# Kernel tuning notes

Measured on AMD Instinct MI355X. Metric: run time of the kernel, lower is better.

Reference implementation:

```python
import jax, jax.numpy as jnp
import numpy as np

N, C, G = 262144, 256, 1024
R = C // 4  # reduction bottleneck


def _linear_w(key, out_dim, in_dim):
    # torch.nn.Linear default init: U(-1/sqrt(in), 1/sqrt(in)), weight shape [out, in]
    bound = 1.0 / np.sqrt(in_dim)
    return jax.random.uniform(key, (out_dim, in_dim), jnp.float32, -bound, bound)


def setup_inputs() -> dict:
    key = jax.random.key(0)
    ks = jax.random.split(key, 8)
    return {
        "x": jax.random.normal(ks[0], (N, C), jnp.float32),
        "glb_w1": _linear_w(ks[1], R, C),
        "glb_a": jnp.full((1,), 0.25, jnp.float32),   # PReLU param (default init 0.25)
        "glb_w2": _linear_w(ks[2], C, R),
        "local_w1": _linear_w(ks[3], R, C),
        "local_a": jnp.full((1,), 0.25, jnp.float32),
        "local_w2": _linear_w(ks[4], C, R),
        "attn_w1": _linear_w(ks[5], R, C),
        "attn_a": jnp.full((1,), 0.25, jnp.float32),
        "attn_w2": _linear_w(ks[6], C, R),
        "batch_idx": jnp.sort(jax.random.randint(ks[7], (N,), 0, G)),
        "num_graphs": G,
    }


def _mlp(h, w1, a, w2):
    # Linear(no bias) -> PReLU -> Linear(no bias)
    z = jnp.einsum('nc,rc->nr', h, w1)
    z = jnp.where(z >= 0, z, a * z)
    return jnp.einsum('nr,cr->nc', z, w2)


def reference(x, glb_w1, glb_a, glb_w2, local_w1, local_a, local_w2,
              attn_w1, attn_a, attn_w2, batch_idx, num_graphs):
    g = _mlp(x, glb_w1, glb_a, glb_w2)                                  # [N, C]
    seg_sum = jax.ops.segment_sum(g, batch_idx, num_segments=num_graphs)  # [G, C]
    cnt = jax.ops.segment_sum(jnp.ones((x.shape[0], 1), x.dtype), batch_idx,
                              num_segments=num_graphs)                  # [G, 1]
    seg_mean = seg_sum / jnp.maximum(cnt, 1.0)  # scatter_mean (0 for empty graphs)
    x_glb = seg_mean[batch_idx]                                          # gather back [N, C]
    loc = _mlp(x, local_w1, local_a, local_w2)                           # [N, C]
    attn = _mlp(loc + x_glb, attn_w1, attn_a, attn_w2)
    return jax.nn.sigmoid(attn)
```

## Files before the change

kernel.cpp:

```cpp
#include <hip/hip_runtime.h>

typedef unsigned short u16;
typedef __attribute__((ext_vector_type(8))) short short8;
typedef __attribute__((ext_vector_type(4))) float f32x4;
typedef __attribute__((ext_vector_type(4))) unsigned short u16x4;
typedef __attribute__((ext_vector_type(2))) unsigned u32x2;

#define NN 262144
#define CC 256
#define RR 64
#define GG 1024

#define SWZ(b, n) ((b) ^ (((n) & 7) << 4))
#define SSWZ(b, r) ((b) ^ (((r) & 7) << 4))


static __device__ __forceinline__ u16 f2bf(float f) {
  unsigned u = __builtin_bit_cast(unsigned, f);
  u += 0x7fffu + ((u >> 16) & 1u);
  return (u16)(u >> 16);
}

static __device__ __forceinline__ unsigned cvt_pk_bf16(float lo, float hi) {
  unsigned r;
  asm("v_cvt_pk_bf16_f32 %0, %1, %2" : "=v"(r) : "v"(lo), "v"(hi));
  return r;
}

static __device__ __forceinline__ void lgkm0() {
  __asm__ volatile("s_waitcnt lgkmcnt(0)" ::: "memory");
}

#define MFMA16(a, b, c) __builtin_amdgcn_mfma_f32_16x16x32_bf16((a), (b), (c), 0, 0, 0)

__global__ void k_prep(const float* __restrict__ a0, const float* __restrict__ a1,
                       const float* __restrict__ a2, const float* __restrict__ a3,
                       const float* __restrict__ a4, const float* __restrict__ a5,
                       u16* __restrict__ dst, float* __restrict__ zbase) {
  int bid = blockIdx.x;
  if (bid < 96) {
    int m = bid >> 4;
    const float* s = (m == 0) ? a0 : (m == 1) ? a1 : (m == 2) ? a2
                   : (m == 3) ? a3 : (m == 4) ? a4 : a5;
    int off = (((bid & 15) << 8) | threadIdx.x) << 2;
    f32x4 v = *(const f32x4*)(s + off);
    u16x4 p;
    p[0] = f2bf(v[0]); p[1] = f2bf(v[1]); p[2] = f2bf(v[2]); p[3] = f2bf(v[3]);
    *(u16x4*)(dst + m * 16384 + off) = p;
  } else {
    int idx = (bid - 96) * 256 + threadIdx.x;
    ((f32x4*)zbase)[idx] = (f32x4){0.f, 0.f, 0.f, 0.f};
  }
}

#define ZBOFF 16384

__global__ __launch_bounds__(256)
__attribute__((amdgpu_waves_per_eu(8, 8))) void k_glb(
    const float* __restrict__ x, const u16* __restrict__ wbf,
    const int* __restrict__ bidx, const float* __restrict__ pa,
    float* __restrict__ seg, int* __restrict__ cnt) {
  __shared__ __align__(16) char smem[20480];
  const int tid = threadIdx.x;
  const int wave = tid >> 6, lane = tid & 63;
  const int low = lane & 15, quad = lane >> 4;
  const int node0 = blockIdx.x << 5;
  const float alpha = pa[0];
  const u16* w1 = wbf;
  const u16* w2 = wbf + 16384;

  const int lbv = bidx[node0 + (lane & 31)];

  const float* xsrc = x + (size_t)node0 * CC;
#pragma unroll
  for (int k = 0; k < 8; k++) {
    int f = k * 1024 + tid * 4;
    f32x4 v = *(const f32x4*)(xsrc + f);
    int node = f >> 8;
    u32x2 p;
    p[0] = cvt_pk_bf16(v[0], v[1]);
    p[1] = cvt_pk_bf16(v[2], v[3]);
    *(u32x2*)(smem + SWZ(node * 512 + (f & 255) * 2, node)) = p;
  }

  if (wave == 0) {
    int cur = __shfl(lbv, 0), rl = 0;
#pragma unroll
    for (int n = 0; n < 32; n++) {
      int b = __shfl(lbv, n);
      if (b != cur) { if (lane == 0) atomicAdd(cnt + cur, rl); rl = 0; cur = b; }
      rl++;
    }
    if (lane == 0) atomicAdd(cnt + cur, rl);
  }
  __syncthreads();

  f32x4 z[2] = {};
  const u16* w1p = w1 + (wave * 16 + low) * CC;
#pragma unroll
  for (int ks = 0; ks < 8; ks++) {
    short8 wa = *(const short8*)(w1p + ks * 32 + quad * 8);
#pragma unroll
    for (int nt = 0; nt < 2; nt++) {
      int node = nt * 16 + low;
      short8 xf = *(const short8*)(smem + SWZ(node * 512 + ks * 64 + quad * 16, node));
      z[nt] = MFMA16(wa, xf, z[nt]);
    }
  }
#pragma unroll
  for (int nt = 0; nt < 2; nt++) {
    float v0 = z[nt][0], v1 = z[nt][1], v2 = z[nt][2], v3 = z[nt][3];
    v0 = v0 >= 0.f ? v0 : alpha * v0;
    v1 = v1 >= 0.f ? v1 : alpha * v1;
    v2 = v2 >= 0.f ? v2 : alpha * v2;
    v3 = v3 >= 0.f ? v3 : alpha * v3;
    int node = nt * 16 + low;
    u32x2 p;
    p[0] = cvt_pk_bf16(v0, v1);
    p[1] = cvt_pk_bf16(v2, v3);
    *(u32x2*)(smem + ZBOFF + SWZ(node * 128 + wave * 32 + quad * 8, node)) = p;
  }
  __syncthreads();

  char* slab = smem + wave * 4096;
#pragma unroll
  for (int nt = 0; nt < 2; nt++) {
    int node = nt * 16 + low;
    f32x4 g[4] = {};
#pragma unroll
    for (int ks2 = 0; ks2 < 2; ks2++) {
      short8 zf = *(const short8*)(smem + ZBOFF + SWZ(node * 128 + ks2 * 64 + quad * 16, node));
#pragma unroll
      for (int mt = 0; mt < 4; mt++) {
        short8 wa = *(const short8*)(w2 + (wave * 64 + mt * 16 + low) * RR + ks2 * 32 + quad * 8);
        g[mt] = MFMA16(wa, zf, g[mt]);
      }
    }
#pragma unroll
    for (int mt = 0; mt < 4; mt++)
      *(f32x4*)(slab + SSWZ(low * 256 + mt * 64 + quad * 16, low)) = g[mt];
    lgkm0();
    float acc = 0.f;
    int cur = __shfl(lbv, nt * 16);
#pragma unroll
    for (int n = 0; n < 16; n++) {
      int b = __shfl(lbv, nt * 16 + n);
      if (b != cur) {
        atomicAdd(seg + (size_t)cur * CC + wave * 64 + lane, acc);
        acc = 0.f; cur = b;
      }
      acc += *(const float*)(slab + SSWZ(n * 256 + lane * 4, n));
    }
    atomicAdd(seg + (size_t)cur * CC + wave * 64 + lane, acc);
    lgkm0();
  }
}

__global__ __launch_bounds__(256)
__attribute__((amdgpu_waves_per_eu(8, 8))) void k_attn(
    const float* __restrict__ x, const u16* __restrict__ wbf,
    const int* __restrict__ bidx, const float* __restrict__ seg,
    const int* __restrict__ cnt,
    const float* __restrict__ pal, const float* __restrict__ paa,
    float* __restrict__ out) {
  __shared__ __align__(16) char smem[20480];
  const int tid = threadIdx.x;
  const int wave = tid >> 6, lane = tid & 63;
  const int low = lane & 15, quad = lane >> 4;
  const int node0 = blockIdx.x << 5;
  const float al = pal[0], aa = paa[0];
  const u16* w1l = wbf + 2 * 16384;
  const u16* w2l = wbf + 3 * 16384;
  const u16* w1a = wbf + 4 * 16384;
  const u16* w2a = wbf + 5 * 16384;

  int bb[2], cc[2];
#pragma unroll
  for (int nt = 0; nt < 2; nt++) bb[nt] = bidx[node0 + nt * 16 + low];
#pragma unroll
  for (int nt = 0; nt < 2; nt++) cc[nt] = cnt[bb[nt]];

  const float* xsrc = x + (size_t)node0 * CC;
#pragma unroll
  for (int k = 0; k < 8; k++) {
    int f = k * 1024 + tid * 4;
    f32x4 v = *(const f32x4*)(xsrc + f);
    int node = f >> 8;
    u32x2 p;
    p[0] = cvt_pk_bf16(v[0], v[1]);
    p[1] = cvt_pk_bf16(v[2], v[3]);
    *(u32x2*)(smem + SWZ(node * 512 + (f & 255) * 2, node)) = p;
  }
  __syncthreads();

  f32x4 z[2] = {};
  const u16* w1p = w1l + (wave * 16 + low) * CC;
#pragma unroll
  for (int ks = 0; ks < 8; ks++) {
    short8 wa = *(const short8*)(w1p + ks * 32 + quad * 8);
#pragma unroll
    for (int nt = 0; nt < 2; nt++) {
      int node = nt * 16 + low;
      short8 xf = *(const short8*)(smem + SWZ(node * 512 + ks * 64 + quad * 16, node));
      z[nt] = MFMA16(wa, xf, z[nt]);
    }
  }
#pragma unroll
  for (int nt = 0; nt < 2; nt++) {
    float v0 = z[nt][0], v1 = z[nt][1], v2 = z[nt][2], v3 = z[nt][3];
    v0 = v0 >= 0.f ? v0 : al * v0;
    v1 = v1 >= 0.f ? v1 : al * v1;
    v2 = v2 >= 0.f ? v2 : al * v2;
    v3 = v3 >= 0.f ? v3 : al * v3;
    int node = nt * 16 + low;
    u32x2 p;
    p[0] = cvt_pk_bf16(v0, v1);
    p[1] = cvt_pk_bf16(v2, v3);
    *(u32x2*)(smem + ZBOFF + SWZ(node * 128 + wave * 32 + quad * 8, node)) = p;
  }
  __syncthreads();

#pragma unroll
  for (int nt = 0; nt < 2; nt++) {
    int node = nt * 16 + low;
    f32x4 loc[4] = {};
#pragma unroll
    for (int ks2 = 0; ks2 < 2; ks2++) {
      short8 zf = *(const short8*)(smem + ZBOFF + SWZ(node * 128 + ks2 * 64 + quad * 16, node));
#pragma unroll
      for (int mt = 0; mt < 4; mt++) {
        short8 wa = *(const short8*)(w2l + (wave * 64 + mt * 16 + low) * RR + ks2 * 32 + quad * 8);
        loc[mt] = MFMA16(wa, zf, loc[mt]);
      }
    }
    const float* srow = seg + (size_t)bb[nt] * CC + wave * 64;
    float inv = (cc[nt] > 0) ? __builtin_amdgcn_rcpf((float)cc[nt]) : 0.0f;
#pragma unroll
    for (int mt = 0; mt < 4; mt++) {
      f32x4 sv = *(const f32x4*)(srow + mt * 16 + quad * 4);
      u32x2 p;
      p[0] = cvt_pk_bf16(fmaf(sv[0], inv, loc[mt][0]),
                         fmaf(sv[1], inv, loc[mt][1]));
      p[1] = cvt_pk_bf16(fmaf(sv[2], inv, loc[mt][2]),
                         fmaf(sv[3], inv, loc[mt][3]));
      *(u32x2*)(smem + SWZ(node * 512 + wave * 128 + mt * 32 + quad * 8, node)) = p;
    }
  }
  __syncthreads();

  f32x4 z2[2] = {};
  const u16* w1pa = w1a + (wave * 16 + low) * CC;
#pragma unroll
  for (int ks = 0; ks < 8; ks++) {
    short8 wa = *(const short8*)(w1pa + ks * 32 + quad * 8);
#pragma unroll
    for (int nt = 0; nt < 2; nt++) {
      int node = nt * 16 + low;
      short8 hf = *(const short8*)(smem + SWZ(node * 512 + ks * 64 + quad * 16, node));
      z2[nt] = MFMA16(wa, hf, z2[nt]);
    }
  }
#pragma unroll
  for (int nt = 0; nt < 2; nt++) {
    float v0 = z2[nt][0], v1 = z2[nt][1], v2 = z2[nt][2], v3 = z2[nt][3];
    v0 = v0 >= 0.f ? v0 : aa * v0;
    v1 = v1 >= 0.f ? v1 : aa * v1;
    v2 = v2 >= 0.f ? v2 : aa * v2;
    v3 = v3 >= 0.f ? v3 : aa * v3;
    int node = nt * 16 + low;
    u32x2 p;
    p[0] = cvt_pk_bf16(v0, v1);
    p[1] = cvt_pk_bf16(v2, v3);
    *(u32x2*)(smem + ZBOFF + SWZ(node * 128 + wave * 32 + quad * 8, node)) = p;
  }
  __syncthreads();

#pragma unroll
  for (int nt = 0; nt < 2; nt++) {
    int node = nt * 16 + low;
    f32x4 o[4] = {};
#pragma unroll
    for (int ks2 = 0; ks2 < 2; ks2++) {
      short8 zf = *(const short8*)(smem + ZBOFF + SWZ(node * 128 + ks2 * 64 + quad * 16, node));
#pragma unroll
      for (int mt = 0; mt < 4; mt++) {
        short8 wa = *(const short8*)(w2a + (wave * 64 + mt * 16 + low) * RR + ks2 * 32 + quad * 8);
        o[mt] = MFMA16(wa, zf, o[mt]);
      }
    }
    float* orow = out + (size_t)(node0 + node) * CC + wave * 64;
#pragma unroll
    for (int mt = 0; mt < 4; mt++) {
#pragma unroll
      for (int i = 0; i < 4; i++)
        o[mt][i] = __builtin_amdgcn_rcpf(1.0f + __expf(-o[mt][i]));
      *(f32x4*)(orow + mt * 16 + quad * 4) = o[mt];
    }
  }
}

extern "C" void kernel_launch(void* const* d_in, const int* in_sizes, int n_in,
                              void* d_out, int out_size, void* d_ws, size_t ws_size,
                              hipStream_t stream) {
  (void)in_sizes; (void)n_in; (void)out_size; (void)ws_size;
  const float* x   = (const float*)d_in[0];
  const float* w1g = (const float*)d_in[1];
  const float* ag  = (const float*)d_in[2];
  const float* w2g = (const float*)d_in[3];
  const float* w1l = (const float*)d_in[4];
  const float* al  = (const float*)d_in[5];
  const float* w2l = (const float*)d_in[6];
  const float* w1a = (const float*)d_in[7];
  const float* aa  = (const float*)d_in[8];
  const float* w2a = (const float*)d_in[9];
  const int* bidx  = (const int*)d_in[10];
  float* out = (float*)d_out;

  u16* wbf   = (u16*)d_ws;
  float* seg = (float*)((char*)d_ws + 196608);
  int* cnt   = (int*)((char*)d_ws + 196608 + 1048576);

  k_prep<<<353, 256, 0, stream>>>(w1g, w2g, w1l, w2l, w1a, w2a, wbf, seg);
  k_glb<<<NN / 32, 256, 0, stream>>>(x, wbf, bidx, ag, seg, cnt);
  k_attn<<<NN / 32, 256, 0, stream>>>(x, wbf, bidx, seg, cnt, al, aa, out);
}
```

Measured before the change: 683.8 us.

## Fuse phases into persistent cooperative kernel with bf16 x cache and prefetch

Replaces the three launches with one persistent cooperative kernel of 1280 blocks that uses grid syncs between weight conversion, the global MLP with segment-sum, and the attention phase. During the global phase each block writes the bf16-converted x tile to workspace, so the attention phase reads half as many bytes instead of re-reading fp32 x. Both tile loops prefetch the next tile's x and batch indices into registers while the current tile computes, and occupancy is pinned to 5 waves per EU. Risks are grid-sync cost, reduced occupancy, and dependence on workspace size, with a three-launch fallback when cooperative launch is unavailable.

```diff
diff --git a/kernel.cpp b/kernel.cpp
--- a/kernel.cpp
+++ b/kernel.cpp
@@ -1,4 +1,7 @@
 #include <hip/hip_runtime.h>
+#include <hip/hip_cooperative_groups.h>
+
+namespace cg = cooperative_groups;
 
 typedef unsigned short u16;
 typedef __attribute__((ext_vector_type(8))) short short8;
@@ -10,10 +13,15 @@
 #define CC 256
 #define RR 64
 #define GG 1024
+#define NTILES 8192
+#define NB 1280
 
 #define SWZ(b, n) ((b) ^ (((n) & 7) << 4))
 #define SSWZ(b, r) ((b) ^ (((r) & 7) << 4))
 
+#define XBFOFF 1249280
+#define XBFSZ  ((size_t)NN * CC * 2)
+#define ZBOFF 16384
 
 static __device__ __forceinline__ u16 f2bf(float f) {
   unsigned u = __builtin_bit_cast(unsigned, f);
@@ -33,268 +41,301 @@
 
 #define MFMA16(a, b, c) __builtin_amdgcn_mfma_f32_16x16x32_bf16((a), (b), (c), 0, 0, 0)
 
-__global__ void k_prep(const float* __restrict__ a0, const float* __restrict__ a1,
-                       const float* __restrict__ a2, const float* __restrict__ a3,
-                       const float* __restrict__ a4, const float* __restrict__ a5,
-                       u16* __restrict__ dst, float* __restrict__ zbase) {
-  int bid = blockIdx.x;
-  if (bid < 96) {
-    int m = bid >> 4;
-    const float* s = (m == 0) ? a0 : (m == 1) ? a1 : (m == 2) ? a2
-                   : (m == 3) ? a3 : (m == 4) ? a4 : a5;
-    int off = (((bid & 15) << 8) | threadIdx.x) << 2;
-    f32x4 v = *(const f32x4*)(s + off);
-    u16x4 p;
-    p[0] = f2bf(v[0]); p[1] = f2bf(v[1]); p[2] = f2bf(v[2]); p[3] = f2bf(v[3]);
-    *(u16x4*)(dst + m * 16384 + off) = p;
-  } else {
-    int idx = (bid - 96) * 256 + threadIdx.x;
-    ((f32x4*)zbase)[idx] = (f32x4){0.f, 0.f, 0.f, 0.f};
-  }
-}
-
-#define ZBOFF 16384
-
 __global__ __launch_bounds__(256)
-__attribute__((amdgpu_waves_per_eu(8, 8))) void k_glb(
-    const float* __restrict__ x, const u16* __restrict__ wbf,
-    const int* __restrict__ bidx, const float* __restrict__ pa,
-    float* __restrict__ seg, int* __restrict__ cnt) {
+__attribute__((amdgpu_waves_per_eu(5, 5))) void k_main(
+    int phase,
+    const float* __restrict__ x, u16* __restrict__ wbf,
+    const float* __restrict__ ws0, const float* __restrict__ ws1,
+    const float* __restrict__ ws2, const float* __restrict__ ws3,
+    const float* __restrict__ ws4, const float* __restrict__ ws5,
+    const int* __restrict__ bidx,
+    const float* __restrict__ pag, const float* __restrict__ pal,
+    const float* __restrict__ paa,
+    float* __restrict__ seg, int* __restrict__ cnt,
+    char* __restrict__ xbf, float* __restrict__ out) {
   __shared__ __align__(16) char smem[20480];
   const int tid = threadIdx.x;
   const int wave = tid >> 6, lane = tid & 63;
   const int low = lane & 15, quad = lane >> 4;
-  const int node0 = blockIdx.x << 5;
-  const float alpha = pa[0];
-  const u16* w1 = wbf;
-  const u16* w2 = wbf + 16384;
-
-  const int lbv = bidx[node0 + (lane & 31)];
-
-  const float* xsrc = x + (size_t)node0 * CC;
-#pragma unroll
-  for (int k = 0; k < 8; k++) {
-    int f = k * 1024 + tid * 4;
-    f32x4 v = *(const f32x4*)(xsrc + f);
-    int node = f >> 8;
-    u32x2 p;
-    p[0] = cvt_pk_bf16(v[0], v[1]);
-    p[1] = cvt_pk_bf16(v[2], v[3]);
-    *(u32x2*)(smem + SWZ(node * 512 + (f & 255) * 2, node)) = p;
-  }
-
-  if (wave == 0) {
-    int cur = __shfl(lbv, 0), rl = 0;
-#pragma unroll
-    for (int n = 0; n < 32; n++) {
-      int b = __shfl(lbv, n);
-      if (b != cur) { if (lane == 0) atomicAdd(cnt + cur, rl); rl = 0; cur = b; }
-      rl++;
-    }
-    if (lane == 0) atomicAdd(cnt + cur, rl);
-  }
-  __syncthreads();
-
-  f32x4 z[2] = {};
-  const u16* w1p = w1 + (wave * 16 + low) * CC;
-#pragma unroll
-  for (int ks = 0; ks < 8; ks++) {
-    short8 wa = *(const short8*)(w1p + ks * 32 + quad * 8);
-#pragma unroll
-    for (int nt = 0; nt < 2; nt++) {
-      int node = nt * 16 + low;
-      short8 xf = *(const short8*)(smem + SWZ(node * 512 + ks * 64 + quad * 16, node));
-      z[nt] = MFMA16(wa, xf, z[nt]);
-    }
-  }
-#pragma unroll
-  for (int nt = 0; nt < 2; nt++) {
-    float v0 = z[nt][0], v1 = z[nt][1], v2 = z[nt][2], v3 = z[nt][3];
-    v0 = v0 >= 0.f ? v0 : alpha * v0;
-    v1 = v1 >= 0.f ? v1 : alpha * v1;
-    v2 = v2 >= 0.f ? v2 : alpha * v2;
-    v3 = v3 >= 0.f ? v3 : alpha * v3;
-    int node = nt * 16 + low;
-    u32x2 p;
-    p[0] = cvt_pk_bf16(v0, v1);
-    p[1] = cvt_pk_bf16(v2, v3);
-    *(u32x2*)(smem + ZBOFF + SWZ(node * 128 + wave * 32 + quad * 8, node)) = p;
-  }
-  __syncthreads();
-
-  char* slab = smem + wave * 4096;
-#pragma unroll
-  for (int nt = 0; nt < 2; nt++) {
-    int node = nt * 16 + low;
-    f32x4 g[4] = {};
-#pragma unroll
-    for (int ks2 = 0; ks2 < 2; ks2++) {
-      short8 zf = *(const short8*)(smem + ZBOFF + SWZ(node * 128 + ks2 * 64 + quad * 16, node));
-#pragma unroll
-      for (int mt = 0; mt < 4; mt++) {
-        short8 wa = *(const short8*)(w2 + (wave * 64 + mt * 16 + low) * RR + ks2 * 32 + quad * 8);
-        g[mt] = MFMA16(wa, zf, g[mt]);
-      }
-    }
-#pragma unroll
-    for (int mt = 0; mt < 4; mt++)
-      *(f32x4*)(slab + SSWZ(low * 256 + mt * 64 + quad * 16, low)) = g[mt];
-    lgkm0();
-    float acc = 0.f;
-    int cur = __shfl(lbv, nt * 16);
-#pragma unroll
-    for (int n = 0; n < 16; n++) {
-      int b = __shfl(lbv, nt * 16 + n);
-      if (b != cur) {
+
+  if (phase == 0 || phase == 3) {
+    int idx = blockIdx.x * 256 + tid;
+    if (idx < 24576) {
+      int m = idx >> 12, o4 = (idx & 4095) << 2;
+      const float* s = (m == 0) ? ws0 : (m == 1) ? ws1 : (m == 2) ? ws2
+                     : (m == 3) ? ws3 : (m == 4) ? ws4 : ws5;
+      f32x4 v = *(const f32x4*)(s + o4);
+      u16x4 p;
+      p[0] = f2bf(v[0]); p[1] = f2bf(v[1]); p[2] = f2bf(v[2]); p[3] = f2bf(v[3]);
+      *(u16x4*)(wbf + m * 16384 + o4) = p;
+    } else if (idx < 24576 + 65792) {
+      ((f32x4*)seg)[idx - 24576] = (f32x4){0.f, 0.f, 0.f, 0.f};
+    }
+  }
+  if (phase == 3) cg::this_grid().sync();
+
+  if (phase == 1 || phase == 3) {
+    const u16* w1 = wbf;
+    const u16* w2 = wbf + 16384;
+    const float alpha = pag[0];
+    f32x4 xn[8];
+    int lbvn = 0;
+    int t0 = blockIdx.x;
+    if (t0 < NTILES) {
+      const float* xs = x + ((size_t)t0 << 5) * CC;
+#pragma unroll
+      for (int k = 0; k < 8; k++) xn[k] = *(const f32x4*)(xs + k * 1024 + tid * 4);
+      lbvn = bidx[(t0 << 5) + (lane & 31)];
+    }
+    for (int t = t0; t < NTILES; t += gridDim.x) {
+      const int lbv = lbvn;
+      char* xtile = xbf ? (xbf + ((size_t)t << 14)) : nullptr;
+#pragma unroll
+      for (int k = 0; k < 8; k++) {
+        int f = k * 1024 + tid * 4;
+        int node = f >> 8;
+        u32x2 p;
+        p[0] = cvt_pk_bf16(xn[k][0], xn[k][1]);
+        p[1] = cvt_pk_bf16(xn[k][2], xn[k][3]);
+        int off = SWZ(node * 512 + (f & 255) * 2, node);
+        *(u32x2*)(smem + off) = p;
+        if (xtile) *(u32x2*)(xtile + off) = p;
+      }
+      __syncthreads();
+      if (t + (int)gridDim.x < NTILES) {
+        const float* xs = x + ((size_t)(t + gridDim.x) << 5) * CC;
+#pragma unroll
+        for (int k = 0; k < 8; k++) xn[k] = *(const f32x4*)(xs + k * 1024 + tid * 4);
+        lbvn = bidx[((t + gridDim.x) << 5) + (lane & 31)];
+      }
+      if (wave == 0) {
+        int cur = __shfl(lbv, 0), rl = 0;
+#pragma unroll
+        for (int n = 0; n < 32; n++) {
+          int b = __shfl(lbv, n);
+          if (b != cur) { if (lane == 0) atomicAdd(cnt + cur, rl); rl = 0; cur = b; }
+          rl++;
+        }
+        if (lane == 0) atomicAdd(cnt + cur, rl);
+      }
+      f32x4 z[2] = {};
+      const u16* w1p = w1 + (wave * 16 + low) * CC;
+#pragma unroll
+      for (int ks = 0; ks < 8; ks++) {
+        short8 wa = *(const short8*)(w1p + ks * 32 + quad * 8);
+#pragma unroll
+        for (int nt = 0; nt < 2; nt++) {
+          int node = nt * 16 + low;
+          short8 xf = *(const short8*)(smem + SWZ(node * 512 + ks * 64 + quad * 16, node));
+          z[nt] = MFMA16(wa, xf, z[nt]);
+        }
+      }
+#pragma unroll
+      for (int nt = 0; nt < 2; nt++) {
+        float v0 = z[nt][0], v1 = z[nt][1], v2 = z[nt][2], v3 = z[nt][3];
+        v0 = v0 >= 0.f ? v0 : alpha * v0;
+        v1 = v1 >= 0.f ? v1 : alpha * v1;
+        v2 = v2 >= 0.f ? v2 : alpha * v2;
+        v3 = v3 >= 0.f ? v3 : alpha * v3;
+        int node = nt * 16 + low;
+        u32x2 p;
+        p[0] = cvt_pk_bf16(v0, v1);
+        p[1] = cvt_pk_bf16(v2, v3);
+        *(u32x2*)(smem + ZBOFF + SWZ(node * 128 + wave * 32 + quad * 8, node)) = p;
+      }
+      __syncthreads();
+      char* slab = smem + wave * 4096;
+#pragma unroll
+      for (int nt = 0; nt < 2; nt++) {
+        int node = nt * 16 + low;
+        f32x4 g[4] = {};
+#pragma unroll
+        for (int ks2 = 0; ks2 < 2; ks2++) {
+          short8 zf = *(const short8*)(smem + ZBOFF + SWZ(node * 128 + ks2 * 64 + quad * 16, node));
+#pragma unroll
+          for (int mt = 0; mt < 4; mt++) {
+            short8 wa = *(const short8*)(w2 + (wave * 64 + mt * 16 + low) * RR + ks2 * 32 + quad * 8);
+            g[mt] = MFMA16(wa, zf, g[mt]);
+          }
+        }
+#pragma unroll
+        for (int mt = 0; mt < 4; mt++)
+          *(f32x4*)(slab + SSWZ(low * 256 + mt * 64 + quad * 16, low)) = g[mt];
+        lgkm0();
+        float acc = 0.f;
+        int cur = __shfl(lbv, nt * 16);
+#pragma unroll
+        for (int n = 0; n < 16; n++) {
+          int b = __shfl(lbv, nt * 16 + n);
+          if (b != cur) {
+            atomicAdd(seg + (size_t)cur * CC + wave * 64 + lane, acc);
+            acc = 0.f; cur = b;
+          }
+          acc += *(const float*)(slab + SSWZ(n * 256 + lane * 4, n));
+        }
         atomicAdd(seg + (size_t)cur * CC + wave * 64 + lane, acc);
-        acc = 0.f; cur = b;
-      }
-      acc += *(const float*)(slab + SSWZ(n * 256 + lane * 4, n));
-    }
-    atomicAdd(seg + (size_t)cur * CC + wave * 64 + lane, acc);
-    lgkm0();
-  }
-}
-
-__global__ __launch_bounds__(256)
-__attribute__((amdgpu_waves_per_eu(8, 8))) void k_attn(
-    const float* __restrict__ x, const u16* __restrict__ wbf,
-    const int* __restrict__ bidx, const float* __restrict__ seg,
-    const int* __restrict__ cnt,
-    const float* __restrict__ pal, const float* __restrict__ paa,
-    float* __restrict__ out) {
-  __shared__ __align__(16) char smem[20480];
-  const int tid = threadIdx.x;
-  const int wave = tid >> 6, lane = tid & 63;
-  const int low = lane & 15, quad = lane >> 4;
-  const int node0 = blockIdx.x << 5;
-  const float al = pal[0], aa = paa[0];
-  const u16* w1l = wbf + 2 * 16384;
-  const u16* w2l = wbf + 3 * 16384;
-  const u16* w1a = wbf + 4 * 16384;
-  const u16* w2a = wbf + 5 * 16384;
-
-  int bb[2], cc[2];
-#pragma unroll
-  for (int nt = 0; nt < 2; nt++) bb[nt] = bidx[node0 + nt * 16 + low];
-#pragma unroll
-  for (int nt = 0; nt < 2; nt++) cc[nt] = cnt[bb[nt]];
-
-  const float* xsrc = x + (size_t)node0 * CC;
-#pragma unroll
-  for (int k = 0; k < 8; k++) {
-    int f = k * 1024 + tid * 4;
-    f32x4 v = *(const f32x4*)(xsrc + f);
-    int node = f >> 8;
-    u32x2 p;
-    p[0] = cvt_pk_bf16(v[0], v[1]);
-    p[1] = cvt_pk_bf16(v[2], v[3]);
-    *(u32x2*)(smem + SWZ(node * 512 + (f & 255) * 2, node)) = p;
-  }
-  __syncthreads();
-
-  f32x4 z[2] = {};
-  const u16* w1p = w1l + (wave * 16 + low) * CC;
-#pragma unroll
-  for (int ks = 0; ks < 8; ks++) {
-    short8 wa = *(const short8*)(w1p + ks * 32 + quad * 8);
-#pragma unroll
-    for (int nt = 0; nt < 2; nt++) {
-      int node = nt * 16 + low;
-      short8 xf = *(const short8*)(smem + SWZ(node * 512 + ks * 64 + quad * 16, node));
-      z[nt] = MFMA16(wa, xf, z[nt]);
-    }
-  }
-#pragma unroll
-  for (int nt = 0; nt < 2; nt++) {
-    float v0 = z[nt][0], v1 = z[nt][1], v2 = z[nt][2], v3 = z[nt][3];
-    v0 = v0 >= 0.f ? v0 : al * v0;
-    v1 = v1 >= 0.f ? v1 : al * v1;
-    v2 = v2 >= 0.f ? v2 : al * v2;
-    v3 = v3 >= 0.f ? v3 : al * v3;
-    int node = nt * 16 + low;
-    u32x2 p;
-    p[0] = cvt_pk_bf16(v0, v1);
-    p[1] = cvt_pk_bf16(v2, v3);
-    *(u32x2*)(smem + ZBOFF + SWZ(node * 128 + wave * 32 + quad * 8, node)) = p;
-  }
-  __syncthreads();
-
-#pragma unroll
-  for (int nt = 0; nt < 2; nt++) {
-    int node = nt * 16 + low;
-    f32x4 loc[4] = {};
-#pragma unroll
-    for (int ks2 = 0; ks2 < 2; ks2++) {
-      short8 zf = *(const short8*)(smem + ZBOFF + SWZ(node * 128 + ks2 * 64 + quad * 16, node));
-#pragma unroll
-      for (int mt = 0; mt < 4; mt++) {
-        short8 wa = *(const short8*)(w2l + (wave * 64 + mt * 16 + low) * RR + ks2 * 32 + quad * 8);
-        loc[mt] = MFMA16(wa, zf, loc[mt]);
-      }
-    }
-    const float* srow = seg + (size_t)bb[nt] * CC + wave * 64;
-    float inv = (cc[nt] > 0) ? __builtin_amdgcn_rcpf((float)cc[nt]) : 0.0f;
-#pragma unroll
-    for (int mt = 0; mt < 4; mt++) {
-      f32x4 sv = *(const f32x4*)(srow + mt * 16 + quad * 4);
-      u32x2 p;
-      p[0] = cvt_pk_bf16(fmaf(sv[0], inv, loc[mt][0]),
-                         fmaf(sv[1], inv, loc[mt][1]));
-      p[1] = cvt_pk_bf16(fmaf(sv[2], inv, loc[mt][2]),
-                         fmaf(sv[3], inv, loc[mt][3]));
-      *(u32x2*)(smem + SWZ(node * 512 + wave * 128 + mt * 32 + quad * 8, node)) = p;
-    }
-  }
-  __syncthreads();
-
-  f32x4 z2[2] = {};
-  const u16* w1pa = w1a + (wave * 16 + low) * CC;
-#pragma unroll
-  for (int ks = 0; ks < 8; ks++) {
-    short8 wa = *(const short8*)(w1pa + ks * 32 + quad * 8);
-#pragma unroll
-    for (int nt = 0; nt < 2; nt++) {
-      int node = nt * 16 + low;
-      short8 hf = *(const short8*)(smem + SWZ(node * 512 + ks * 64 + quad * 16, node));
-      z2[nt] = MFMA16(wa, hf, z2[nt]);
-    }
-  }
-#pragma unroll
-  for (int nt = 0; nt < 2; nt++) {
-    float v0 = z2[nt][0], v1 = z2[nt][1], v2 = z2[nt][2], v3 = z2[nt][3];
-    v0 = v0 >= 0.f ? v0 : aa * v0;
-    v1 = v1 >= 0.f ? v1 : aa * v1;
-    v2 = v2 >= 0.f ? v2 : aa * v2;
-    v3 = v3 >= 0.f ? v3 : aa * v3;
-    int node = nt * 16 + low;
-    u32x2 p;
-    p[0] = cvt_pk_bf16(v0, v1);
-    p[1] = cvt_pk_bf16(v2, v3);
-    *(u32x2*)(smem + ZBOFF + SWZ(node * 128 + wave * 32 + quad * 8, node)) = p;
-  }
-  __syncthreads();
-
-#pragma unroll
-  for (int nt = 0; nt < 2; nt++) {
-    int node = nt * 16 + low;
-    f32x4 o[4] = {};
-#pragma unroll
-    for (int ks2 = 0; ks2 < 2; ks2++) {
-      short8 zf = *(const short8*)(smem + ZBOFF + SWZ(node * 128 + ks2 * 64 + quad * 16, node));
-#pragma unroll
-      for (int mt = 0; mt < 4; mt++) {
-        short8 wa = *(const short8*)(w2a + (wave * 64 + mt * 16 + low) * RR + ks2 * 32 + quad * 8);
-        o[mt] = MFMA16(wa, zf, o[mt]);
-      }
-    }
-    float* orow = out + (size_t)(node0 + node) * CC + wave * 64;
-#pragma unroll
-    for (int mt = 0; mt < 4; mt++) {
-#pragma unroll
-      for (int i = 0; i < 4; i++)
-        o[mt][i] = __builtin_amdgcn_rcpf(1.0f + __expf(-o[mt][i]));
-      *(f32x4*)(orow + mt * 16 + quad * 4) = o[mt];
+        lgkm0();
+      }
+      __syncthreads();
+    }
+  }
+  if (phase == 3) cg::this_grid().sync();
+
+  if (phase == 2 || phase == 3) {
+    const u16* w1l = wbf + 2 * 16384;
+    const u16* w2l = wbf + 3 * 16384;
+    const u16* w1a = wbf + 4 * 16384;
+    const u16* w2a = wbf + 5 * 16384;
+    const float al = pal[0], aa = paa[0];
+    f32x4 xn2[4];
+    int bbn[2] = {0, 0}, ccn[2] = {0, 0};
+    int t0 = blockIdx.x;
+    if (t0 < NTILES) {
+      if (xbf) {
+        const char* gs = xbf + ((size_t)t0 << 14);
+#pragma unroll
+        for (int j = 0; j < 4; j++) xn2[j] = *(const f32x4*)(gs + tid * 16 + j * 4096);
+      }
+#pragma unroll
+      for (int nt = 0; nt < 2; nt++) bbn[nt] = bidx[(t0 << 5) + nt * 16 + low];
+#pragma unroll
+      for (int nt = 0; nt < 2; nt++) ccn[nt] = cnt[bbn[nt]];
+    }
+    for (int t = t0; t < NTILES; t += gridDim.x) {
+      const int node0 = t << 5;
+      int bb[2] = {bbn[0], bbn[1]};
+      int cc2[2] = {ccn[0], ccn[1]};
+      if (xbf) {
+#pragma unroll
+        for (int j = 0; j < 4; j++)
+          *(f32x4*)(smem + tid * 16 + j * 4096) = xn2[j];
+      } else {
+        const float* xs = x + (size_t)node0 * CC;
+#pragma unroll
+        for (int k = 0; k < 8; k++) {
+          int f = k * 1024 + tid * 4;
+          f32x4 v = *(const f32x4*)(xs + f);
+          int node = f >> 8;
+          u32x2 p;
+          p[0] = cvt_pk_bf16(v[0], v[1]);
+          p[1] = cvt_pk_bf16(v[2], v[3]);
+          *(u32x2*)(smem + SWZ(node * 512 + (f & 255) * 2, node)) = p;
+        }
+      }
+      __syncthreads();
+      if (t + (int)gridDim.x < NTILES) {
+        int tn = t + gridDim.x;
+        if (xbf) {
+          const char* gs = xbf + ((size_t)tn << 14);
+#pragma unroll
+          for (int j = 0; j < 4; j++) xn2[j] = *(const f32x4*)(gs + tid * 16 + j * 4096);
+        }
+#pragma unroll
+        for (int nt = 0; nt < 2; nt++) bbn[nt] = bidx[(tn << 5) + nt * 16 + low];
+#pragma unroll
+        for (int nt = 0; nt < 2; nt++) ccn[nt] = cnt[bbn[nt]];
+      }
+      f32x4 z[2] = {};
+      const u16* w1p = w1l + (wave * 16 + low) * CC;
+#pragma unroll
+      for (int ks = 0; ks < 8; ks++) {
+        short8 wa = *(const short8*)(w1p + ks * 32 + quad * 8);
+#pragma unroll
+        for (int nt = 0; nt < 2; nt++) {
+          int node = nt * 16 + low;
+          short8 xf = *(const short8*)(smem + SWZ(node * 512 + ks * 64 + quad * 16, node));
+          z[nt] = MFMA16(wa, xf, z[nt]);
+        }
+      }
+#pragma unroll
+      for (int nt = 0; nt < 2; nt++) {
+        float v0 = z[nt][0], v1 = z[nt][1], v2 = z[nt][2], v3 = z[nt][3];
+        v0 = v0 >= 0.f ? v0 : al * v0;
+        v1 = v1 >= 0.f ? v1 : al * v1;
+        v2 = v2 >= 0.f ? v2 : al * v2;
+        v3 = v3 >= 0.f ? v3 : al * v3;
+        int node = nt * 16 + low;
+        u32x2 p;
+        p[0] = cvt_pk_bf16(v0, v1);
+        p[1] = cvt_pk_bf16(v2, v3);
+        *(u32x2*)(smem + ZBOFF + SWZ(node * 128 + wave * 32 + quad * 8, node)) = p;
+      }
+      __syncthreads();
+#pragma unroll
+      for (int nt = 0; nt < 2; nt++) {
+        int node = nt * 16 + low;
+        f32x4 loc[4] = {};
+#pragma unroll
+        for (int ks2 = 0; ks2 < 2; ks2++) {
+          short8 zf = *(const short8*)(smem + ZBOFF + SWZ(node * 128 + ks2 * 64 + quad * 16, node));
+#pragma unroll
+          for (int mt = 0; mt < 4; mt++) {
+            short8 wa = *(const short8*)(w2l + (wave * 64 + mt * 16 + low) * RR + ks2 * 32 + quad * 8);
+            loc[mt] = MFMA16(wa, zf, loc[mt]);
+          }
+        }
+        const float* srow = seg + (size_t)bb[nt] * CC + wave * 64;
+        float inv = (cc2[nt] > 0) ? __builtin_amdgcn_rcpf((float)cc2[nt]) : 0.0f;
+#pragma unroll
+        for (int mt = 0; mt < 4; mt++) {
+          f32x4 sv = *(const f32x4*)(srow + mt * 16 + quad * 4);
+          u32x2 p;
+          p[0] = cvt_pk_bf16(fmaf(sv[0], inv, loc[mt][0]),
+                             fmaf(sv[1], inv, loc[mt][1]));
+          p[1] = cvt_pk_bf16(fmaf(sv[2], inv, loc[mt][2]),
+                             fmaf(sv[3], inv, loc[mt][3]));
+          *(u32x2*)(smem + SWZ(node * 512 + wave * 128 + mt * 32 + quad * 8, node)) = p;
+        }
+      }
+      __syncthreads();
+      f32x4 z2[2] = {};
+      const u16* w1pa = w1a + (wave * 16 + low) * CC;
+#pragma unroll
+      for (int ks = 0; ks < 8; ks++) {
+        short8 wa = *(const short8*)(w1pa + ks * 32 + quad * 8);
+#pragma unroll
+        for (int nt = 0; nt < 2; nt++) {
+          int node = nt * 16 + low;
+          short8 hf = *(const short8*)(smem + SWZ(node * 512 + ks * 64 + quad * 16, node));
+          z2[nt] = MFMA16(wa, hf, z2[nt]);
+        }
+      }
+#pragma unroll
+      for (int nt = 0; nt < 2; nt++) {
+        float v0 = z2[nt][0], v1 = z2[nt][1], v2 = z2[nt][2], v3 = z2[nt][3];
+        v0 = v0 >= 0.f ? v0 : aa * v0;
+        v1 = v1 >= 0.f ? v1 : aa * v1;
+        v2 = v2 >= 0.f ? v2 : aa * v2;
+        v3 = v3 >= 0.f ? v3 : aa * v3;
+        int node = nt * 16 + low;
+        u32x2 p;
+        p[0] = cvt_pk_bf16(v0, v1);
+        p[1] = cvt_pk_bf16(v2, v3);
+        *(u32x2*)(smem + ZBOFF + SWZ(node * 128 + wave * 32 + quad * 8, node)) = p;
+      }
+      __syncthreads();
+#pragma unroll
+      for (int nt = 0; nt < 2; nt++) {
+        int node = nt * 16 + low;
+        f32x4 o[4] = {};
+#pragma unroll
+        for (int ks2 = 0; ks2 < 2; ks2++) {
+          short8 zf = *(const short8*)(smem + ZBOFF + SWZ(node * 128 + ks2 * 64 + quad * 16, node));
+#pragma unroll
+          for (int mt = 0; mt < 4; mt++) {
+            short8 wa = *(const short8*)(w2a + (wave * 64 + mt * 16 + low) * RR + ks2 * 32 + quad * 8);
+            o[mt] = MFMA16(wa, zf, o[mt]);
+          }
+        }
+        float* orow = out + (size_t)(node0 + node) * CC + wave * 64;
+#pragma unroll
+        for (int mt = 0; mt < 4; mt++) {
+#pragma unroll
+          for (int i = 0; i < 4; i++)
+            o[mt][i] = __builtin_amdgcn_rcpf(1.0f + __expf(-o[mt][i]));
+          *(f32x4*)(orow + mt * 16 + quad * 4) = o[mt];
+        }
+      }
     }
   }
 }
@@ -302,7 +343,7 @@
 extern "C" void kernel_launch(void* const* d_in, const int* in_sizes, int n_in,
                               void* d_out, int out_size, void* d_ws, size_t ws_size,
                               hipStream_t stream) {
-  (void)in_sizes; (void)n_in; (void)out_size; (void)ws_size;
+  (void)in_sizes; (void)n_in; (void)out_size;
   const float* x   = (const float*)d_in[0];
   const float* w1g = (const float*)d_in[1];
   const float* ag  = (const float*)d_in[2];
@@ -319,8 +360,28 @@
   u16* wbf   = (u16*)d_ws;
   float* seg = (float*)((char*)d_ws + 196608);
   int* cnt   = (int*)((char*)d_ws + 196608 + 1048576);
-
-  k_prep<<<353, 256, 0, stream>>>(w1g, w2g, w1l, w2l, w1a, w2a, wbf, seg);
-  k_glb<<<NN / 32, 256, 0, stream>>>(x, wbf, bidx, ag, seg, cnt);
-  k_attn<<<NN / 32, 256, 0, stream>>>(x, wbf, bidx, seg, cnt, al, aa, out);
-}
+  char* xbf  = (ws_size >= (size_t)XBFOFF + XBFSZ) ? ((char*)d_ws + XBFOFF) : nullptr;
+
+  static int coop = -1;
+  if (coop < 0) {
+    int mb = 0;
+    hipError_t e = hipOccupancyMaxActiveBlocksPerMultiprocessor(&mb, k_main, 256, 0);
+    coop = (e == hipSuccess && mb >= 5) ? 1 : 0;
+  }
+
+  int ph = 3;
+  void* args[] = {&ph, &x, &wbf, &w1g, &w2g, &w1l, &w2l, &w1a, &w2a,
+                  &bidx, &ag, &al, &aa, &seg, &cnt, &xbf, &out};
+  if (coop) {
+    hipError_t e = hipLaunchCooperativeKernel((const void*)k_main, dim3(NB),
+                                              dim3(256), args, 0, stream);
+    if (e == hipSuccess) return;
+    coop = 0;
+  }
+  k_main<<<NB, 256, 0, stream>>>(0, x, wbf, w1g, w2g, w1l, w2l, w1a, w2a,
+                                 bidx, ag, al, aa, seg, cnt, xbf, out);
+  k_main<<<NB, 256, 0, stream>>>(1, x, wbf, w1g, w2g, w1l, w2l, w1a, w2a,
+                                 bidx, ag, al, aa, seg, cnt, xbf, out);
+  k_main<<<NB, 256, 0, stream>>>(2, x, wbf, w1g, w2g, w1l, w2l, w1a, w2a,
+                                 bidx, ag, al, aa, seg, cnt, xbf, out);
+}
```

Result: slower. 797.5 us (+16.6%).
